# Performance work log

Measured on AMD Instinct MI355X. Metric: run time of the kernel, lower is better.

The kernel has to match this reference:

```python
import jax, jax.numpy as jnp
import numpy as np

LENS = 11          # odd aperture size (lens_mask init arg)
PAD = LENS // 2    # ReplicationPad2d(lens // 2)


def _distance_kernel(k):
    # k x k Euclidean distance from the kernel center
    c = k // 2
    ii, jj = np.meshgrid(np.arange(k), np.arange(k), indexing="ij")
    return np.sqrt((ii - c) ** 2 + (jj - c) ** 2).astype(np.float32)


def _lens_shape_mask(k):
    # circular aperture: 1 inside the disk of radius k//2
    return (_distance_kernel(k) <= k // 2).astype(np.float32)


def setup_inputs() -> dict:
    key = jax.random.key(0)
    kx, kl = jax.random.split(key)
    # RGBD input: channels 0..2 = color, channel 3 = relative disparity
    x = jax.random.normal(kx, (4, 4, 512, 512), dtype=jnp.float32)
    # per-image lens strength; scaled so splat radii span the full aperture
    lens_effects = jax.random.uniform(kl, (4, 1), dtype=jnp.float32) * 8.0
    return {
        "x": x,
        "lens_effects": lens_effects,
        "diskernel": jnp.asarray(_distance_kernel(LENS)),
        "lens_mask": jnp.asarray(_lens_shape_mask(LENS)),
    }


def _scatter_render(x, lens_effects, diskernel, lens_mask):
    """Depth-aware scatter (splat) bokeh blur.

    Each source pixel p splats its color onto every pixel within its circle of
    confusion radius r_p = clip(|disp_p| * lens_effect, 0, lens//2), with splat
    energy g_p = 1/(pi*r_p^2 + 1) (sharp pixels dominate).  Destinations
    normalize by the accumulated weight.  Implemented as the equivalent gather:
    out[q] = sum_o m_o * [r(q+o) >= d_o] * g(q+o) * rgb(q+o) / (same with rgb=1),
    scanning over the LENS*LENS offsets so no K^2-sized tensor is materialized.
    """
    B, C, H, W = x.shape
    rgb, disp = x[:, :3], x[:, 3:4]
    r = jnp.clip(jnp.abs(disp) * lens_effects[:, :, None, None], 0.0, float(PAD))
    g = 1.0 / (jnp.pi * r * r + 1.0)   # per-source splat energy (B,1,H,W)
    s = rgb * g                         # pre-scaled color (B,3,H,W)

    pad = ((0, 0), (0, 0), (PAD, PAD), (PAD, PAD))
    s_p = jnp.pad(s, pad, mode="edge")  # replication padding
    g_p = jnp.pad(g, pad, mode="edge")
    r_p = jnp.pad(r, pad, mode="edge")

    di = jnp.repeat(jnp.arange(LENS), LENS)
    dj = jnp.tile(jnp.arange(LENS), LENS)
    dists = diskernel.reshape(-1)
    masks = lens_mask.reshape(-1)

    def step(carry, inp):
        num, den = carry
        i, j, dist, mask = inp
        src_s = jax.lax.dynamic_slice(s_p, (0, 0, i, j), (B, 3, H, W))
        src_g = jax.lax.dynamic_slice(g_p, (0, 0, i, j), (B, 1, H, W))
        src_r = jax.lax.dynamic_slice(r_p, (0, 0, i, j), (B, 1, H, W))
        # coverage: source's circle of confusion reaches this destination
        cover = jax.lax.stop_gradient((src_r >= dist).astype(src_r.dtype))
        wm = mask * cover
        return (num + wm * src_s, den + wm * src_g), None

    init = (jnp.zeros((B, 3, H, W), x.dtype), jnp.zeros((B, 1, H, W), x.dtype))
    (num, den), _ = jax.lax.scan(step, init, (di, dj, dists, masks))
    # den > 0 always: the center offset (d=0, m=1) always covers itself
    return num / den


def reference(x, lens_effects, diskernel, lens_mask):
    return _scatter_render(x, lens_effects, diskernel, lens_mask)
```

## Files before the change

kernel.cpp:

```cpp
#include <hip/hip_runtime.h>

#define HH 512
#define WW 512
#define BB 4
#define TILE 16
#define HALO 5
#define LT (TILE + 2 * HALO)
#define PI_F 3.14159265358979323846f

__global__ __launch_bounds__(256) void Scatter_Rendering_87101936763449_kernel(
    const float* __restrict__ x, const float* __restrict__ lens,
    const float* __restrict__ dk, float* __restrict__ out) {
    __shared__ float4 sg[LT * LT];
    __shared__ float  sr[LT * LT];

    const int b  = blockIdx.z;
    const int bx = blockIdx.x * TILE;
    const int by = blockIdx.y * TILE;
    const int t  = threadIdx.x;

    const float le = lens[b];
    const float* xb = x + (size_t)b * 4 * HH * WW;

    for (int i = t; i < LT * LT; i += 256) {
        int ly = i / LT, lx = i - ly * LT;
        int gy = by + ly - HALO; gy = gy < 0 ? 0 : (gy > HH - 1 ? HH - 1 : gy);
        int gx = bx + lx - HALO; gx = gx < 0 ? 0 : (gx > WW - 1 ? WW - 1 : gx);
        int gi = gy * WW + gx;
        float d  = xb[3 * HH * WW + gi];
        float r  = fminf(fabsf(d) * le, (float)HALO);
        float pr = PI_F * r;
        float g  = 1.0f / (pr * r + 1.0f);
        sr[i] = r;
        sg[i] = make_float4(xb[gi] * g, xb[HH * WW + gi] * g, xb[2 * HH * WW + gi] * g, g);
    }

    float distv[26];
#pragma unroll
    for (int a = 0; a <= 5; ++a) {
#pragma unroll
        for (int c = a; c <= 5; ++c) {
            int d2 = a * a + c * c;
            if (d2 <= 25) distv[d2] = dk[(5 + a) * 11 + (5 + c)];
        }
    }

    __syncthreads();

    const int tx = t & (TILE - 1);
    const int ty = t >> 4;
    const int base = ty * LT + tx;

    float n0 = 0.f, n1 = 0.f, n2 = 0.f, den = 0.f;
#pragma unroll
    for (int di = 0; di < 11; ++di) {
#pragma unroll
        for (int dj = 0; dj < 11; ++dj) {
            const int d2 = (di - 5) * (di - 5) + (dj - 5) * (dj - 5);
            if (d2 > 25) continue;
            const float dist = distv[d2];
            const int idx = base + di * LT + dj;
            float  r = sr[idx];
            float4 v = sg[idx];
            float wm = (r >= dist) ? 1.0f : 0.0f;
            n0  = fmaf(wm, v.x, n0);
            n1  = fmaf(wm, v.y, n1);
            n2  = fmaf(wm, v.z, n2);
            den = fmaf(wm, v.w, den);
        }
    }

    const float inv = 1.0f / den;
    const size_t o = (size_t)b * 3 * HH * WW + (size_t)(by + ty) * WW + (bx + tx);
    out[o]               = n0 * inv;
    out[o + HH * WW]     = n1 * inv;
    out[o + 2 * HH * WW] = n2 * inv;
}

extern "C" void kernel_launch(void* const* d_in, const int* in_sizes, int n_in,
                              void* d_out, int out_size, void* d_ws, size_t ws_size,
                              hipStream_t stream) {
    const float* x    = (const float*)d_in[0];
    const float* lens = (const float*)d_in[1];
    const float* dk   = (const float*)d_in[2];
    float* out = (float*)d_out;

    dim3 grid(WW / TILE, HH / TILE, BB);
    dim3 block(256);
    hipLaunchKernelGGL(Scatter_Rendering_87101936763449_kernel, grid, block, 0, stream,
                       x, lens, dk, out);
}
```

Before: 100.8 us.

## Use 32x32 tiles with 4-row register blocking and column-wise LDS reuse

Grows the spatial tile from 16x16 to 32x32 and has each thread compute four vertically adjacent output pixels. For each horizontal offset it loads a column of radius and premultiplied color values from shared memory into registers once and reuses them across vertical offsets and the four outputs. This cuts shared-memory reads per output and shrinks the halo overhead per tile. In exchange it uses more registers per thread and more shared memory per block, which may reduce occupancy, and it adds padded row strides in shared memory.

```diff
diff --git a/kernel.cpp b/kernel.cpp
--- a/kernel.cpp
+++ b/kernel.cpp
@@ -3,16 +3,18 @@
 #define HH 512
 #define WW 512
 #define BB 4
-#define TILE 16
+#define TILE 32
 #define HALO 5
 #define LT (TILE + 2 * HALO)
+#define SGS 43
+#define SRS 43
 #define PI_F 3.14159265358979323846f
 
 __global__ __launch_bounds__(256) void Scatter_Rendering_87101936763449_kernel(
     const float* __restrict__ x, const float* __restrict__ lens,
     const float* __restrict__ dk, float* __restrict__ out) {
-    __shared__ float4 sg[LT * LT];
-    __shared__ float  sr[LT * LT];
+    __shared__ float4 sg[LT * SGS];
+    __shared__ float  sr[LT * SRS];
 
     const int b  = blockIdx.z;
     const int bx = blockIdx.x * TILE;
@@ -29,10 +31,10 @@
         int gi = gy * WW + gx;
         float d  = xb[3 * HH * WW + gi];
         float r  = fminf(fabsf(d) * le, (float)HALO);
-        float pr = PI_F * r;
-        float g  = 1.0f / (pr * r + 1.0f);
-        sr[i] = r;
-        sg[i] = make_float4(xb[gi] * g, xb[HH * WW + gi] * g, xb[2 * HH * WW + gi] * g, g);
+        float g  = 1.0f / (PI_F * r * r + 1.0f);
+        sr[ly * SRS + lx] = r;
+        sg[ly * SGS + lx] = make_float4(xb[gi] * g, xb[HH * WW + gi] * g,
+                                        xb[2 * HH * WW + gi] * g, g);
     }
 
     float distv[26];
@@ -47,34 +49,57 @@
 
     __syncthreads();
 
-    const int tx = t & (TILE - 1);
-    const int ty = t >> 4;
-    const int base = ty * LT + tx;
+    const int tx   = t & 31;
+    const int tyq  = t >> 5;
+    const int yloc = tyq * 4;
 
-    float n0 = 0.f, n1 = 0.f, n2 = 0.f, den = 0.f;
+    const int DIMIN[11] = {5, 2, 1, 1, 1, 0, 1, 1, 1, 2, 5};
+    const int DIMAX[11] = {5, 8, 9, 9, 9, 10, 9, 9, 9, 8, 5};
+
+    float acc[4][4];
 #pragma unroll
-    for (int di = 0; di < 11; ++di) {
+    for (int p = 0; p < 4; ++p)
 #pragma unroll
-        for (int dj = 0; dj < 11; ++dj) {
+        for (int c = 0; c < 4; ++c) acc[p][c] = 0.f;
+
+#pragma unroll
+    for (int dj = 0; dj < 11; ++dj) {
+        const int lo = DIMIN[dj], hi = DIMAX[dj];
+        float  rr[14];
+        float4 vv[14];
+#pragma unroll
+        for (int k = 0; k <= 13; ++k) {
+            if (k > hi - lo + 3) continue;
+            const int row = yloc + lo + k;
+            rr[k] = sr[row * SRS + tx + dj];
+            vv[k] = sg[row * SGS + tx + dj];
+        }
+#pragma unroll
+        for (int di = 0; di <= 10; ++di) {
+            if (di < lo || di > hi) continue;
             const int d2 = (di - 5) * (di - 5) + (dj - 5) * (dj - 5);
-            if (d2 > 25) continue;
             const float dist = distv[d2];
-            const int idx = base + di * LT + dj;
-            float  r = sr[idx];
-            float4 v = sg[idx];
-            float wm = (r >= dist) ? 1.0f : 0.0f;
-            n0  = fmaf(wm, v.x, n0);
-            n1  = fmaf(wm, v.y, n1);
-            n2  = fmaf(wm, v.z, n2);
-            den = fmaf(wm, v.w, den);
+#pragma unroll
+            for (int p = 0; p < 4; ++p) {
+                const float  r = rr[di - lo + p];
+                const float4 v = vv[di - lo + p];
+                const float wm = (r >= dist) ? 1.0f : 0.0f;
+                acc[p][0] = fmaf(wm, v.x, acc[p][0]);
+                acc[p][1] = fmaf(wm, v.y, acc[p][1]);
+                acc[p][2] = fmaf(wm, v.z, acc[p][2]);
+                acc[p][3] = fmaf(wm, v.w, acc[p][3]);
+            }
         }
     }
 
-    const float inv = 1.0f / den;
-    const size_t o = (size_t)b * 3 * HH * WW + (size_t)(by + ty) * WW + (bx + tx);
-    out[o]               = n0 * inv;
-    out[o + HH * WW]     = n1 * inv;
-    out[o + 2 * HH * WW] = n2 * inv;
+#pragma unroll
+    for (int p = 0; p < 4; ++p) {
+        const float inv = 1.0f / acc[p][3];
+        const size_t o = (size_t)b * 3 * HH * WW + (size_t)(by + yloc + p) * WW + (bx + tx);
+        out[o]               = acc[p][0] * inv;
+        out[o + HH * WW]     = acc[p][1] * inv;
+        out[o + 2 * HH * WW] = acc[p][2] * inv;
+    }
 }
 
 extern "C" void kernel_launch(void* const* d_in, const int* in_sizes, int n_in,
```

Result: slower. 118.2 us (+17.3%).
